# Kernel optimization log

Hardware: AMD Instinct MI355X
Metric: run time of the kernel (lower is better)

Reference implementation:

```python
import jax, jax.numpy as jnp
import numpy as np

N_PARENT = 16384
N_CHILD = 8 * N_PARENT  # nearest upsample, nempty=False: 8 children per parent
C = 128
K = 27  # 3x3x3 octree conv stencil


def setup_inputs() -> dict:
    key = jax.random.key(0)
    k1, k2, k3, k4 = jax.random.split(key, 4)
    x = jax.random.normal(k1, (N_PARENT, C), dtype=jnp.float32)
    # conv weight per stencil offset, fan-in scaled init
    w = jax.random.normal(k2, (K, C, C), dtype=jnp.float32) / np.sqrt(K * C)
    b = jnp.zeros((C,), dtype=jnp.float32)
    # neighbor table at depth+1; -1 marks missing neighbors (zero-padded)
    neigh = jax.random.randint(k3, (N_CHILD, K), -1, N_CHILD, dtype=jnp.int32)
    return {"x": x, "w": w, "b": b, "neigh": neigh}


def reference(x, w, b, neigh):
    # OctreeUpsample(nearest, nempty=False): copy each parent feature to its
    # 8 contiguous children at depth+1.
    xu = jnp.repeat(x, 8, axis=0)  # [N_child, C]
    # OctreeConv: gather 27 neighbors (missing -> 0), then GEMM + bias.
    valid = neigh >= 0  # [N_child, 27]
    g = jnp.where(valid[..., None], xu[jnp.clip(neigh, 0)], 0.0)  # [N_child, 27, C]
    out = jnp.einsum('nkc,kcd->nd', g, w) + b  # [N_child, C]
    return out
```

## Files before the change

kernel.cpp:

```cpp
#include <hip/hip_runtime.h>
#include <hip/hip_bf16.h>

#define N_PARENT 16384
#define N_CHILD (8 * N_PARENT)
#define CC 128
#define KK 27

#define BM 128
#define BK 64
#define NSTAGE (KK * 2)

#define XB_OFF 0
#define XB_ELEMS (N_PARENT * CC)
#define WT_OFF XB_ELEMS
#define WT_ELEMS (KK * CC * CC)
#define ZR_OFF (WT_OFF + WT_ELEMS)
#define ZR_ELEMS 128

typedef __attribute__((ext_vector_type(8))) __bf16 bf16x8;
typedef __attribute__((ext_vector_type(4))) float f32x4;

__device__ __forceinline__ void gll16(const void* g, void* l) {
  __builtin_amdgcn_global_load_lds(
      (const __attribute__((address_space(1))) unsigned int*)g,
      (__attribute__((address_space(3))) unsigned int*)l,
      16, 0, 0);
}

__global__ void prep_kernel(const float* __restrict__ x,
                            const float* __restrict__ w,
                            __hip_bfloat16* __restrict__ ws) {
  const int stride = gridDim.x * blockDim.x;
  const int tid = blockIdx.x * blockDim.x + threadIdx.x;
  for (int i = tid; i < XB_ELEMS; i += stride)
    ws[XB_OFF + i] = __float2bfloat16(x[i]);
  for (int j = tid; j < WT_ELEMS; j += stride) {
    const int k = j / (CC * CC);
    const int rem = j - k * CC * CC;
    const int d = rem >> 7;
    const int c = rem & 127;
    ws[WT_OFF + j] = __float2bfloat16(w[k * CC * CC + c * CC + d]);
  }
  if (tid < ZR_ELEMS) ws[ZR_OFF + tid] = __float2bfloat16(0.0f);
}

__global__ __launch_bounds__(256, 2) void upconv_kernel(
    const int* __restrict__ neigh,
    const __hip_bfloat16* __restrict__ ws,
    const float* __restrict__ bias,
    float* __restrict__ out) {
  __shared__ __align__(16) __hip_bfloat16 As[2][BM * BK];
  __shared__ __align__(16) __hip_bfloat16 Bs[2][CC * BK];
  __shared__ short ridx[BM * KK];

  const __hip_bfloat16* xb = ws + XB_OFF;
  const __hip_bfloat16* wT = ws + WT_OFF;
  const __hip_bfloat16* zr = ws + ZR_OFF;

  const int tid = threadIdx.x;
  const int wv = tid >> 6;
  const int l = tid & 63;
  const int wr = wv >> 1;
  const int wc = wv & 1;
  const int row0 = blockIdx.x * BM;

  for (int j = tid; j < BM * KK; j += 256) {
    const int nv = neigh[row0 * KK + j];
    ridx[j] = (short)((nv >= 0) ? (nv >> 3) : -1);
  }
  __syncthreads();

  const int lr = l & 15;
  const int lk = (l >> 4) * 8;
  const int lrow = l >> 3;
  const int scol = ((l & 7) ^ lrow) * 8;

  f32x4 acc[4][4] = {};

  auto stage = [&](int buf, int s) {
    const int k = s >> 1;
    const int hOff = (s & 1) << 6;
#pragma unroll
    for (int i = 0; i < 4; ++i) {
      const int rg = wv * 32 + i * 8;
      const int rr = rg + lrow;
      const int ix = (int)ridx[rr * KK + k];
      const __hip_bfloat16* ga =
          (ix >= 0) ? (xb + (size_t)ix * CC + hOff + scol) : (zr + scol);
      gll16(ga, &As[buf][rg * BK]);
      const __hip_bfloat16* gb =
          wT + (size_t)k * (CC * CC) + (size_t)rr * CC + hOff + scol;
      gll16(gb, &Bs[buf][rg * BK]);
    }
  };

  auto compute = [&](int buf) {
    const int sw = (lr & 7) * 8;
#pragma unroll
    for (int kc = 0; kc < 2; ++kc) {
      const int ce = (kc * 32 + lk) ^ sw;
      bf16x8 a[4], bb[4];
#pragma unroll
      for (int m = 0; m < 4; ++m)
        a[m] = *reinterpret_cast<const bf16x8*>(
            &As[buf][(wr * 64 + m * 16 + lr) * BK + ce]);
#pragma unroll
      for (int n = 0; n < 4; ++n)
        bb[n] = *reinterpret_cast<const bf16x8*>(
            &Bs[buf][(wc * 64 + n * 16 + lr) * BK + ce]);
#pragma unroll
      for (int m = 0; m < 4; ++m)
#pragma unroll
        for (int n = 0; n < 4; ++n)
          acc[m][n] =
              __builtin_amdgcn_mfma_f32_16x16x32_bf16(a[m], bb[n], acc[m][n],
                                                      0, 0, 0);
    }
  };

  stage(0, 0);
  __syncthreads();
  int cur = 0;
#pragma unroll 2
  for (int s = 0; s < NSTAGE; ++s) {
    if (s + 1 < NSTAGE) stage(cur ^ 1, s + 1);
    compute(cur);
    __syncthreads();
    cur ^= 1;
  }

  float bv[4];
#pragma unroll
  for (int n = 0; n < 4; ++n) bv[n] = bias[wc * 64 + n * 16 + lr];
  const int rbase = row0 + wr * 64 + (l >> 4) * 4;
#pragma unroll
  for (int m = 0; m < 4; ++m)
#pragma unroll
    for (int n = 0; n < 4; ++n)
#pragma unroll
      for (int q = 0; q < 4; ++q)
        out[(size_t)(rbase + m * 16 + q) * CC + wc * 64 + n * 16 + lr] =
            acc[m][n][q] + bv[n];
}

extern "C" void kernel_launch(void* const* d_in, const int* in_sizes, int n_in,
                              void* d_out, int out_size, void* d_ws,
                              size_t ws_size, hipStream_t stream) {
  const float* x = (const float*)d_in[0];
  const float* w = (const float*)d_in[1];
  const float* b = (const float*)d_in[2];
  const int* neigh = (const int*)d_in[3];
  __hip_bfloat16* ws = (__hip_bfloat16*)d_ws;
  float* out = (float*)d_out;

  hipLaunchKernelGGL(prep_kernel, dim3(512), dim3(256), 0, stream, x, w, ws);
  hipLaunchKernelGGL(upconv_kernel, dim3(N_CHILD / BM), dim3(256), 0, stream,
                     neigh, ws, b, out);
}
```

Measured before the change: 150.0 us.

## Stream weight fragments from global into registers, triple-buffer gathered A tiles

The weight tile is no longer staged through LDS. Each wave loads its B fragments directly from global memory into double-buffered registers, while gathered activation rows use a 3-slot LDS ring with BK=32 and hand-placed vmcnt waits and raw barriers. Missing neighbors now point at a fixed zero row index (ZR_ROW) instead of a branch. The change also raises occupancy to 3 blocks per CU and sets MFMA priority. This aims to cut LDS traffic and shared-memory footprint and to hide gather latency. In exchange there are more stages, more global loads of B per wave, and fragile manual wait counting.

```diff
diff --git a/kernel.cpp b/kernel.cpp
--- a/kernel.cpp
+++ b/kernel.cpp
@@ -7,8 +7,9 @@
 #define KK 27
 
 #define BM 128
-#define BK 64
-#define NSTAGE (KK * 2)
+#define BN 128
+#define BK 32
+#define NSTAGE 108
 
 #define XB_OFF 0
 #define XB_ELEMS (N_PARENT * CC)
@@ -16,6 +17,7 @@
 #define WT_ELEMS (KK * CC * CC)
 #define ZR_OFF (WT_OFF + WT_ELEMS)
 #define ZR_ELEMS 128
+#define ZR_ROW 19840
 
 typedef __attribute__((ext_vector_type(8))) __bf16 bf16x8;
 typedef __attribute__((ext_vector_type(4))) float f32x4;
@@ -44,18 +46,15 @@
   if (tid < ZR_ELEMS) ws[ZR_OFF + tid] = __float2bfloat16(0.0f);
 }
 
-__global__ __launch_bounds__(256, 2) void upconv_kernel(
+#define WAITN(n) asm volatile("s_waitcnt vmcnt(" #n ")" ::: "memory")
+
+__global__ __launch_bounds__(256, 3) void upconv_kernel(
     const int* __restrict__ neigh,
     const __hip_bfloat16* __restrict__ ws,
     const float* __restrict__ bias,
     float* __restrict__ out) {
-  __shared__ __align__(16) __hip_bfloat16 As[2][BM * BK];
-  __shared__ __align__(16) __hip_bfloat16 Bs[2][CC * BK];
-  __shared__ short ridx[BM * KK];
-
-  const __hip_bfloat16* xb = ws + XB_OFF;
-  const __hip_bfloat16* wT = ws + WT_OFF;
-  const __hip_bfloat16* zr = ws + ZR_OFF;
+  __shared__ __align__(16) __hip_bfloat16 As[3][BM * BK];
+  __shared__ unsigned short ridx[BM * KK];
 
   const int tid = threadIdx.x;
   const int wv = tid >> 6;
@@ -66,67 +65,89 @@
 
   for (int j = tid; j < BM * KK; j += 256) {
     const int nv = neigh[row0 * KK + j];
-    ridx[j] = (short)((nv >= 0) ? (nv >> 3) : -1);
+    ridx[j] = (unsigned short)((nv >= 0) ? (nv >> 3) : ZR_ROW);
   }
   __syncthreads();
 
   const int lr = l & 15;
-  const int lk = (l >> 4) * 8;
-  const int lrow = l >> 3;
-  const int scol = ((l & 7) ^ lrow) * 8;
+  const int coE = ((l >> 4) ^ ((lr >> 1) & 3)) * 8;
+  const int g16 = l >> 2;
+  const int lch = ((l & 3) ^ ((l >> 3) & 3)) * 16;
+
+  const char* xbB = (const char*)(ws + XB_OFF);
+  const char* wTB =
+      (const char*)(ws + WT_OFF) + (wc * 64 + lr) * 256 + (l >> 4) * 16;
+  const int riB0 = (wv * 32 + g16) * KK;
+  const int riB1 = (wv * 32 + 16 + g16) * KK;
 
   f32x4 acc[4][4] = {};
+  bf16x8 aF[2][4], bF[2][4];
+  int r0[2], r1[2], r2[2];
 
-  auto stage = [&](int buf, int s) {
-    const int k = s >> 1;
-    const int hOff = (s & 1) << 6;
+  auto ridload = [&](int* r, int tap) {
+    const int T = tap > 26 ? 26 : tap;
+    r[0] = ((int)ridx[riB0 + T]) << 8;
+    r[1] = ((int)ridx[riB1 + T]) << 8;
+  };
+  auto stageA = [&](int slot, int qb, const int* r) {
+    gll16(xbB + r[0] + qb + lch, &As[slot][(wv * 32) * BK]);
+    gll16(xbB + r[1] + qb + lch, &As[slot][(wv * 32 + 16) * BK]);
+  };
+  auto loadB = [&](bf16x8* b, const char* base) {
 #pragma unroll
-    for (int i = 0; i < 4; ++i) {
-      const int rg = wv * 32 + i * 8;
-      const int rr = rg + lrow;
-      const int ix = (int)ridx[rr * KK + k];
-      const __hip_bfloat16* ga =
-          (ix >= 0) ? (xb + (size_t)ix * CC + hOff + scol) : (zr + scol);
-      gll16(ga, &As[buf][rg * BK]);
-      const __hip_bfloat16* gb =
-          wT + (size_t)k * (CC * CC) + (size_t)rr * CC + hOff + scol;
-      gll16(gb, &Bs[buf][rg * BK]);
-    }
+    for (int n = 0; n < 4; ++n)
+      b[n] = *reinterpret_cast<const bf16x8*>(base + n * 4096);
+  };
+  auto fragA = [&](bf16x8* a, int slot) {
+#pragma unroll
+    for (int m = 0; m < 4; ++m)
+      a[m] = *reinterpret_cast<const bf16x8*>(
+          &As[slot][(wr * 64 + m * 16 + lr) * BK + coE]);
+  };
+  auto mfma16 = [&](const bf16x8* a, const bf16x8* b) {
+    __builtin_amdgcn_s_setprio(1);
+#pragma unroll
+    for (int m = 0; m < 4; ++m)
+#pragma unroll
+      for (int n = 0; n < 4; ++n)
+        acc[m][n] = __builtin_amdgcn_mfma_f32_16x16x32_bf16(a[m], b[n],
+                                                            acc[m][n], 0, 0, 0);
+    __builtin_amdgcn_s_setprio(0);
   };
 
-  auto compute = [&](int buf) {
-    const int sw = (lr & 7) * 8;
+  ridload(r2, 0);
+  loadB(bF[0], wTB);
+  stageA(0, 0, r2);
+  stageA(1, 64, r2);
+  WAITN(2);
+  __syncthreads();
+  fragA(aF[0], 0);
+  asm volatile("s_waitcnt lgkmcnt(0)" ::: "memory");
+
+  const char* wTt = wTB;
+  for (int t = 0; t < 9; ++t) {
 #pragma unroll
-    for (int kc = 0; kc < 2; ++kc) {
-      const int ce = (kc * 32 + lk) ^ sw;
-      bf16x8 a[4], bb[4];
-#pragma unroll
-      for (int m = 0; m < 4; ++m)
-        a[m] = *reinterpret_cast<const bf16x8*>(
-            &As[buf][(wr * 64 + m * 16 + lr) * BK + ce]);
-#pragma unroll
-      for (int n = 0; n < 4; ++n)
-        bb[n] = *reinterpret_cast<const bf16x8*>(
-            &Bs[buf][(wc * 64 + n * 16 + lr) * BK + ce]);
-#pragma unroll
-      for (int m = 0; m < 4; ++m)
-#pragma unroll
-        for (int n = 0; n < 4; ++n)
-          acc[m][n] =
-              __builtin_amdgcn_mfma_f32_16x16x32_bf16(a[m], bb[n], acc[m][n],
-                                                      0, 0, 0);
+    for (int j = 0; j < 12; ++j) {
+      const int s = 12 * t + j;
+      if (s + 1 < NSTAGE)
+        loadB(bF[(j + 1) & 1],
+              wTt + ((j + 1) >> 2) * 32768 + ((j + 1) & 3) * 64);
+      if (s + 2 < NSTAGE) {
+        const int* rs = (j < 2) ? r2 : (j < 6) ? r0 : (j < 10) ? r1 : r2;
+        stageA((j + 2) % 3, ((j + 2) & 3) * 64, rs);
+      }
+      if (s < NSTAGE - 2)       WAITN(6);
+      else if (s == NSTAGE - 2) WAITN(4);
+      else                      WAITN(0);
+      __builtin_amdgcn_s_barrier();
+      if (s + 1 < NSTAGE) fragA(aF[(j + 1) & 1], (j + 1) % 3);
+      if (j == 0)      ridload(r0, 3 * t + 1);
+      else if (j == 4) ridload(r1, 3 * t + 2);
+      else if (j == 8) ridload(r2, 3 * t + 3);
+      mfma16(aF[j & 1], bF[j & 1]);
+      asm volatile("s_waitcnt lgkmcnt(0)" ::: "memory");
     }
-  };
-
-  stage(0, 0);
-  __syncthreads();
-  int cur = 0;
-#pragma unroll 2
-  for (int s = 0; s < NSTAGE; ++s) {
-    if (s + 1 < NSTAGE) stage(cur ^ 1, s + 1);
-    compute(cur);
-    __syncthreads();
-    cur ^= 1;
+    wTt += 98304;
   }
 
   float bv[4];
```

Result: slower. 242.4 us (+61.6%).
